# Performance work log

Measured on AMD Instinct MI355X. Metric: run time of the kernel, lower is better.

## Reference

```python
import jax, jax.numpy as jnp
import numpy as np

NUM_EXPERTS = 256
TOP_K = 8
N_GROUP = 8
TOPK_GROUP = 4
ROUTED_SCALING = 2.5
EXPERTS_PER_GROUP = NUM_EXPERTS // N_GROUP  # 32


def setup_inputs() -> dict:
    key = jax.random.key(0)
    k1, k2, k3 = jax.random.split(key, 3)
    hidden_states = jax.random.normal(k1, (8192, 7168), dtype=jnp.float32)
    weight = jax.random.normal(k2, (NUM_EXPERTS, 7168), dtype=jnp.float32) * 0.02
    e_score_correction_bias = jax.random.normal(k3, (NUM_EXPERTS,), dtype=jnp.float32) * 0.1
    return {
        "hidden_states": hidden_states,
        "weight": weight,
        "e_score_correction_bias": e_score_correction_bias,
    }


def reference(hidden_states, weight, e_score_correction_bias):
    # Router logits: [T, E]
    router_logits = jnp.einsum("th,eh->te", hidden_states, weight)
    scores = jax.nn.sigmoid(router_logits)
    scores_for_choice = scores + e_score_correction_bias  # [T, E]

    T = scores_for_choice.shape[0]
    # Group-limited selection (noaux_tc): group score = sum of top-2 experts in group
    grouped = scores_for_choice.reshape(T, N_GROUP, EXPERTS_PER_GROUP)
    group_top2, _ = jax.lax.top_k(grouped, 2)            # [T, G, 2]
    group_scores = group_top2.sum(axis=-1)               # [T, G]
    _, group_idx = jax.lax.top_k(group_scores, TOPK_GROUP)  # [T, topk_group]
    group_mask = jax.nn.one_hot(group_idx, N_GROUP, dtype=scores.dtype).max(axis=1)  # [T, G]
    expert_mask = jnp.repeat(group_mask, EXPERTS_PER_GROUP, axis=-1)  # [T, E]
    masked_scores = scores_for_choice * expert_mask

    # Final top-k experts; routing weights gathered from raw sigmoid scores
    _, selected_experts = jax.lax.top_k(masked_scores, TOP_K)         # [T, K] int32
    routing_weights = jnp.take_along_axis(scores, selected_experts, axis=-1)  # [T, K]
    routing_weights = routing_weights / (routing_weights.sum(axis=-1, keepdims=True) + 1e-20)
    routing_weights = routing_weights * ROUTED_SCALING
    return routing_weights, selected_experts
```

## Files before the change

### kernel.cpp

```cpp
#include <hip/hip_runtime.h>
#include <math.h>
#include <stdint.h>

#define T_TOK 8192
#define NEXP  256
#define HD    7168
#define PLANE ((size_t)T_TOK * NEXP)
#define SCALE 4096.0f
#define INV_S2 (1.0f / 16777216.0f)
#define BM 256
#define BK 32
#define NSTEP_TOT (HD / BK)
#define BIMG_STEP 32768

typedef _Float16 h8  __attribute__((ext_vector_type(8)));
typedef float f32x16 __attribute__((ext_vector_type(16)));
typedef __attribute__((address_space(3))) uint8_t       lds_t;
typedef __attribute__((address_space(1))) const uint8_t gbl_t;

__global__ __launch_bounds__(256) void wconv(const float* __restrict__ W,
                                             _Float16* __restrict__ img) {
  const int cc  = blockIdx.x * 256 + threadIdx.x;
  const int t   = cc >> 11;
  const int c   = cc & 2047;
  const int hl  = c >> 10;
  const int rem = c & 1023;
  const int row = rem >> 2;
  const int sp  = rem & 3;
  const int sl  = sp ^ ((row >> 1) & 3);
  const int k   = t * BK + sl * 8;

  const float* src = W + (size_t)row * HD + k;
  const float4 v0 = *(const float4*)src;
  const float4 v1 = *(const float4*)(src + 4);
  const float xs[8] = {v0.x, v0.y, v0.z, v0.w, v1.x, v1.y, v1.z, v1.w};
  h8 out;
#pragma unroll
  for (int j = 0; j < 8; ++j) {
    const float v = xs[j] * SCALE;
    const _Float16 hh = (_Float16)v;
    out[j] = hl ? (_Float16)(v - (float)hh) : hh;
  }
  *(h8*)(img + (size_t)cc * 8) = out;
}

__global__ __launch_bounds__(512, 2) void router_gemm(
    const float* __restrict__ X, const _Float16* __restrict__ img,
    float* __restrict__ partial, int S) {
  __shared__ __align__(1024) _Float16 As[2][2][BM][BK];
  __shared__ __align__(1024) _Float16 Bs[2][2][NEXP][BK];

  const int tid = threadIdx.x;
  const int id  = blockIdx.x;
  const int sb  = id % S;
  const int mb  = id / S;

  const int row0  = mb * BM;
  const int nstep = (HD / S) / BK;
  const int tbase = sb * nstep;

  const int lane = tid & 63, wv = tid >> 6;
  const int wm = wv >> 2, wn = wv & 3;
  const int r31 = lane & 31, kg = lane >> 5;

  const int sm = tid >> 1;
  const int sk = tid & 1;

  const float* Ap = X + (size_t)(row0 + sm) * HD + tbase * BK + sk * 16;
  const uint8_t* imgB = (const uint8_t*)img + (size_t)tbase * BIMG_STEP + tid * 16;

  f32x16 acc[4][2];
#pragma unroll
  for (int i = 0; i < 4; ++i)
#pragma unroll
    for (int j = 0; j < 2; ++j) acc[i][j] = (f32x16)(0.f);

#define LOAD_A(t)                                                              \
  {                                                                            \
    const float* ap = Ap + (size_t)(t) * BK;                                   \
    a0 = *(const float4*)(ap);                                                 \
    a1 = *(const float4*)(ap + 4);                                             \
    a2 = *(const float4*)(ap + 8);                                             \
    a3 = *(const float4*)(ap + 12);                                            \
  }

#define STAGE_B2(t, b, i0)                                                     \
  {                                                                            \
    const uint8_t* g = imgB + (size_t)(t) * BIMG_STEP;                         \
    uint8_t* l = (uint8_t*)&Bs[b][0][0][0] + tid * 16;                         \
    __builtin_amdgcn_global_load_lds((gbl_t*)(uintptr_t)(g + (i0) * 8192),     \
                                     (lds_t*)(uintptr_t)(l + (i0) * 8192), 16, 0, 0); \
    __builtin_amdgcn_global_load_lds((gbl_t*)(uintptr_t)(g + ((i0) + 1) * 8192), \
                                     (lds_t*)(uintptr_t)(l + ((i0) + 1) * 8192), 16, 0, 0); \
  }

#define CVT_WRITE_A(b)                                                         \
  {                                                                            \
    const float xs[16] = {a0.x, a0.y, a0.z, a0.w, a1.x, a1.y, a1.z, a1.w,      \
                          a2.x, a2.y, a2.z, a2.w, a3.x, a3.y, a3.z, a3.w};     \
    h8 hv0, hv1, lv0, lv1;                                                     \
    _Pragma("unroll")                                                          \
    for (int j = 0; j < 8; ++j) {                                              \
      const float v = xs[j] * SCALE;                                           \
      const _Float16 hh = (_Float16)v;                                         \
      hv0[j] = hh; lv0[j] = (_Float16)(v - (float)hh);                         \
    }                                                                          \
    _Pragma("unroll")                                                          \
    for (int j = 0; j < 8; ++j) {                                              \
      const float v = xs[8 + j] * SCALE;                                       \
      const _Float16 hh = (_Float16)v;                                         \
      hv1[j] = hh; lv1[j] = (_Float16)(v - (float)hh);                         \
    }                                                                          \
    const int s0 = (sk * 2) ^ ((sm >> 1) & 3);                                 \
    const int s1 = (sk * 2 + 1) ^ ((sm >> 1) & 3);                             \
    *(h8*)&As[b][0][sm][s0 * 8] = hv0;                                         \
    *(h8*)&As[b][0][sm][s1 * 8] = hv1;                                         \
    *(h8*)&As[b][1][sm][s0 * 8] = lv0;                                         \
    *(h8*)&As[b][1][sm][s1 * 8] = lv1;                                         \
  }

#define READ_B(ks, dst)                                                        \
  _Pragma("unroll")                                                            \
  for (int ni = 0; ni < 2; ++ni)                                               \
    _Pragma("unroll")                                                          \
    for (int pl = 0; pl < 2; ++pl) {                                           \
      const int col = wn * 64 + ni * 32 + r31;                                 \
      const int sp  = ((ks) * 2 + kg) ^ ((col >> 1) & 3);                      \
      dst[ni][pl] = *(const h8*)&Bs[cur][pl][col][sp * 8];                     \
    }

#define READ_A(ks, mbase, dst)                                                 \
  _Pragma("unroll")                                                            \
  for (int mi = 0; mi < 2; ++mi)                                               \
    _Pragma("unroll")                                                          \
    for (int pl = 0; pl < 2; ++pl) {                                           \
      const int row = wm * 128 + ((mbase) + mi) * 32 + r31;                    \
      const int sp  = ((ks) * 2 + kg) ^ ((row >> 1) & 3);                      \
      dst[mi][pl] = *(const h8*)&As[cur][pl][row][sp * 8];                     \
    }

#define MFMA12(aF, bF, mbase)                                                  \
  __builtin_amdgcn_s_setprio(1);                                               \
  _Pragma("unroll")                                                            \
  for (int mi = 0; mi < 2; ++mi)                                               \
    _Pragma("unroll")                                                          \
    for (int ni = 0; ni < 2; ++ni)                                             \
      acc[(mbase) + mi][ni] = __builtin_amdgcn_mfma_f32_32x32x16_f16(          \
          aF[mi][0], bF[ni][0], acc[(mbase) + mi][ni], 0, 0, 0);               \
  _Pragma("unroll")                                                            \
  for (int mi = 0; mi < 2; ++mi)                                               \
    _Pragma("unroll")                                                          \
    for (int ni = 0; ni < 2; ++ni)                                             \
      acc[(mbase) + mi][ni] = __builtin_amdgcn_mfma_f32_32x32x16_f16(          \
          aF[mi][1], bF[ni][0], acc[(mbase) + mi][ni], 0, 0, 0);               \
  _Pragma("unroll")                                                            \
  for (int mi = 0; mi < 2; ++mi)                                               \
    _Pragma("unroll")                                                          \
    for (int ni = 0; ni < 2; ++ni)                                             \
      acc[(mbase) + mi][ni] = __builtin_amdgcn_mfma_f32_32x32x16_f16(          \
          aF[mi][0], bF[ni][1], acc[(mbase) + mi][ni], 0, 0, 0);               \
  __builtin_amdgcn_s_setprio(0);

#define FENCE asm volatile("" ::: "memory");
#define BAR   __builtin_amdgcn_s_barrier();
#define WAITL0 asm volatile("s_waitcnt lgkmcnt(0)" ::: "memory"); __builtin_amdgcn_sched_barrier(0);

  {
    float4 a0, a1, a2, a3;
    LOAD_A(0);
    STAGE_B2(0, 0, 0);
    STAGE_B2(0, 0, 2);
    asm volatile("s_waitcnt vmcnt(4)" ::: "memory");
    CVT_WRITE_A(0);
    asm volatile("s_waitcnt vmcnt(0) lgkmcnt(0)" ::: "memory");
    BAR;
  }

  for (int t = 0; t < nstep; ++t) {
    const int cur = t & 1;
    const int nxt = cur ^ 1;
    const bool more = (t + 1 < nstep);

    h8 b0[2][2], b1[2][2], aA[2][2], aB[2][2];
    float4 a0, a1, a2, a3;

    READ_B(0, b0);
    READ_A(0, 0, aA);
    if (more) LOAD_A(t + 1);
    FENCE; BAR; WAITL0;
    MFMA12(aA, b0, 0);
    FENCE; BAR;

    READ_A(0, 2, aB);
    if (more) STAGE_B2(t + 1, nxt, 0);
    FENCE; BAR; WAITL0;
    MFMA12(aB, b0, 2);
    FENCE; BAR;

    READ_B(1, b1);
    READ_A(1, 0, aA);
    if (more) STAGE_B2(t + 1, nxt, 2);
    FENCE; BAR; WAITL0;
    MFMA12(aA, b1, 0);
    FENCE; BAR;

    READ_A(1, 2, aB);
    if (more) {
      asm volatile("s_waitcnt vmcnt(4)" ::: "memory");
      __builtin_amdgcn_sched_barrier(0);
      CVT_WRITE_A(nxt);
    }
    asm volatile("s_waitcnt lgkmcnt(0)" ::: "memory");
    __builtin_amdgcn_sched_barrier(0);
    BAR;
    MFMA12(aB, b1, 2);
    if (more) asm volatile("s_waitcnt vmcnt(0)" ::: "memory");
    FENCE; BAR;
  }

  float* base = partial + (size_t)sb * PLANE;
#pragma unroll
  for (int mi = 0; mi < 4; ++mi)
#pragma unroll
    for (int ni = 0; ni < 2; ++ni) {
      const int col = wn * 64 + ni * 32 + r31;
#pragma unroll
      for (int reg = 0; reg < 16; ++reg) {
        const int rr  = (reg & 3) + 8 * (reg >> 2) + 4 * kg;
        const int row = row0 + wm * 128 + mi * 32 + rr;
        base[(size_t)row * NEXP + col] = acc[mi][ni][reg];
      }
    }
}

__global__ __launch_bounds__(256) void gate_kernel(const float* __restrict__ logits,
                                                   const float* __restrict__ bias,
                                                   float* __restrict__ out_w,
                                                   float* __restrict__ out_e, int S) {
    const int wave = threadIdx.x >> 6;
    const int lane = threadIdx.x & 63;
    const int t = blockIdx.x * 4 + wave;
    if (t >= T_TOK) return;

    float l4[4] = {0.f, 0.f, 0.f, 0.f};
    for (int s = 0; s < S; ++s) {
        const float4 v = *(const float4*)(&logits[(size_t)s * PLANE + (size_t)t * NEXP + lane * 4]);
        l4[0] += v.x; l4[1] += v.y; l4[2] += v.z; l4[3] += v.w;
    }
    const float4 bv = *(const float4*)(&bias[lane * 4]);

    float s4[4], c[4];
#pragma unroll
    for (int j = 0; j < 4; ++j) s4[j] = 1.f / (1.f + expf(-l4[j] * INV_S2));
    c[0] = s4[0] + bv.x;
    c[1] = s4[1] + bv.y;
    c[2] = s4[2] + bv.z;
    c[3] = s4[3] + bv.w;

    float a = fmaxf(c[0], c[1]), b = fminf(c[0], c[1]);
    float d = fmaxf(c[2], c[3]), e = fminf(c[2], c[3]);
    float m1 = fmaxf(a, d);
    float m2 = fmaxf(fminf(a, d), fmaxf(b, e));
#pragma unroll
    for (int off = 1; off < 8; off <<= 1) {
        const float o1 = __shfl_xor(m1, off);
        const float o2 = __shfl_xor(m2, off);
        const float n1 = fmaxf(m1, o1);
        const float n2 = fmaxf(fminf(m1, o1), fmaxf(m2, o2));
        m1 = n1; m2 = n2;
    }
    const float gs = m1 + m2;
    const int   g  = lane >> 3;

    int rank = 0;
#pragma unroll
    for (int gg = 0; gg < 8; ++gg) {
        const float og = __shfl(gs, gg * 8);
        rank += (og > gs) || (og == gs && gg < g);
    }
    const bool gsel = rank < 4;

    float v[4];
#pragma unroll
    for (int j = 0; j < 4; ++j) v[j] = gsel ? c[j] : 0.0f;

    float selw = 0.f;
    int   seli = 0;
    float wsum = 0.f;

#pragma unroll
    for (int k = 0; k < 8; ++k) {
        float bvv = v[0]; int bi = lane * 4; float br = s4[0];
#pragma unroll
        for (int j = 1; j < 4; ++j) {
            if (v[j] > bvv) { bvv = v[j]; bi = lane * 4 + j; br = s4[j]; }
        }
#pragma unroll
        for (int off = 32; off > 0; off >>= 1) {
            const float ov = __shfl_xor(bvv, off);
            const int   oi = __shfl_xor(bi, off);
            const float orr = __shfl_xor(br, off);
            if (ov > bvv || (ov == bvv && oi < bi)) { bvv = ov; bi = oi; br = orr; }
        }
        if (lane == k) { selw = br; seli = bi; }
        wsum += br;
        const int rem = bi - lane * 4;
#pragma unroll
        for (int j = 0; j < 4; ++j)
            if (rem == j) v[j] = -INFINITY;
    }

    if (lane < 8) {
        const float w = selw / (wsum + 1e-20f) * 2.5f;
        out_w[(size_t)t * 8 + lane] = w;
        out_e[(size_t)t * 8 + lane] = (float)seli;
    }
}

extern "C" void kernel_launch(void* const* d_in, const int* in_sizes, int n_in,
                              void* d_out, int out_size, void* d_ws, size_t ws_size,
                              hipStream_t stream) {
    const float* X    = (const float*)d_in[0];
    const float* W    = (const float*)d_in[1];
    const float* bias = (const float*)d_in[2];
    float* out = (float*)d_out;

    _Float16* img = (_Float16*)d_ws;
    const size_t woff = (size_t)NSTEP_TOT * BIMG_STEP;
    float* partial = (float*)((char*)d_ws + woff);

    int S = 1;
    if (ws_size >= woff + 8 * PLANE * sizeof(float)) S = 8;
    else if (ws_size >= woff + 4 * PLANE * sizeof(float)) S = 4;
    else if (ws_size >= woff + 2 * PLANE * sizeof(float)) S = 2;

    wconv<<<dim3(NSTEP_TOT * 2048 / 256), 256, 0, stream>>>(W, img);
    router_gemm<<<dim3((T_TOK / BM) * S), 512, 0, stream>>>(X, img, partial, S);
    gate_kernel<<<dim3(T_TOK / 4), 256, 0, stream>>>(partial, bias, out, out + (size_t)T_TOK * 8, S);
}
```

Baseline: 135.2 us.

## Collapse per-step barriers into one and issue all LDS reads up front

Restructures the main GEMM k-loop so each step has a single workgroup barrier at the top instead of eight barrier points. All A and B fragment reads from LDS are issued early, and partial lgkmcnt waits interleave them with the four MFMA groups. The four B global-to-LDS loads are issued together in one batch. The aim is to cut barrier stalls and expose more overlap between LDS reads, global loads and MFMA work. In exchange it uses more fragment registers and depends on hand-counted waitcnt values being correct for the double-buffered LDS.

```diff
diff --git a/kernel.cpp b/kernel.cpp
--- a/kernel.cpp
+++ b/kernel.cpp
@@ -17,6 +17,8 @@
 typedef float f32x16 __attribute__((ext_vector_type(16)));
 typedef __attribute__((address_space(3))) uint8_t       lds_t;
 typedef __attribute__((address_space(1))) const uint8_t gbl_t;
+
+#define SB __builtin_amdgcn_sched_barrier(0);
 
 __global__ __launch_bounds__(256) void wconv(const float* __restrict__ W,
                                              _Float16* __restrict__ img) {
@@ -84,14 +86,14 @@
     a3 = *(const float4*)(ap + 12);                                            \
   }
 
-#define STAGE_B2(t, b, i0)                                                     \
+#define STAGE_B4(t, b)                                                         \
   {                                                                            \
     const uint8_t* g = imgB + (size_t)(t) * BIMG_STEP;                         \
     uint8_t* l = (uint8_t*)&Bs[b][0][0][0] + tid * 16;                         \
-    __builtin_amdgcn_global_load_lds((gbl_t*)(uintptr_t)(g + (i0) * 8192),     \
-                                     (lds_t*)(uintptr_t)(l + (i0) * 8192), 16, 0, 0); \
-    __builtin_amdgcn_global_load_lds((gbl_t*)(uintptr_t)(g + ((i0) + 1) * 8192), \
-                                     (lds_t*)(uintptr_t)(l + ((i0) + 1) * 8192), 16, 0, 0); \
+    _Pragma("unroll")                                                          \
+    for (int i = 0; i < 4; ++i)                                                \
+      __builtin_amdgcn_global_load_lds((gbl_t*)(uintptr_t)(g + i * 8192),      \
+                                       (lds_t*)(uintptr_t)(l + i * 8192), 16, 0, 0); \
   }
 
 #define CVT_WRITE_A(b)                                                         \
@@ -161,19 +163,12 @@
           aF[mi][0], bF[ni][1], acc[(mbase) + mi][ni], 0, 0, 0);               \
   __builtin_amdgcn_s_setprio(0);
 
-#define FENCE asm volatile("" ::: "memory");
-#define BAR   __builtin_amdgcn_s_barrier();
-#define WAITL0 asm volatile("s_waitcnt lgkmcnt(0)" ::: "memory"); __builtin_amdgcn_sched_barrier(0);
-
   {
     float4 a0, a1, a2, a3;
-    LOAD_A(0);
-    STAGE_B2(0, 0, 0);
-    STAGE_B2(0, 0, 2);
-    asm volatile("s_waitcnt vmcnt(4)" ::: "memory");
+    LOAD_A(0); SB;
+    STAGE_B4(0, 0); SB;
+    asm volatile("s_waitcnt vmcnt(4)" ::: "memory"); SB;
     CVT_WRITE_A(0);
-    asm volatile("s_waitcnt vmcnt(0) lgkmcnt(0)" ::: "memory");
-    BAR;
   }
 
   for (int t = 0; t < nstep; ++t) {
@@ -181,41 +176,42 @@
     const int nxt = cur ^ 1;
     const bool more = (t + 1 < nstep);
 
-    h8 b0[2][2], b1[2][2], aA[2][2], aB[2][2];
     float4 a0, a1, a2, a3;
+    h8 b0[2][2], b1[2][2], aP[2][2], aQ[2][2], aR[2][2], aS[2][2];
+
+    if (more) { LOAD_A(t + 1); }
+    SB;
+    if (more) { asm volatile("s_waitcnt vmcnt(2) lgkmcnt(0)" ::: "memory"); }
+    else      { asm volatile("s_waitcnt vmcnt(0) lgkmcnt(0)" ::: "memory"); }
+    SB;
+    __builtin_amdgcn_s_barrier();
 
     READ_B(0, b0);
-    READ_A(0, 0, aA);
-    if (more) LOAD_A(t + 1);
-    FENCE; BAR; WAITL0;
-    MFMA12(aA, b0, 0);
-    FENCE; BAR;
-
-    READ_A(0, 2, aB);
-    if (more) STAGE_B2(t + 1, nxt, 0);
-    FENCE; BAR; WAITL0;
-    MFMA12(aB, b0, 2);
-    FENCE; BAR;
-
+    READ_A(0, 0, aP);
+    READ_A(0, 2, aQ);
+    SB;
     READ_B(1, b1);
-    READ_A(1, 0, aA);
-    if (more) STAGE_B2(t + 1, nxt, 2);
-    FENCE; BAR; WAITL0;
-    MFMA12(aA, b1, 0);
-    FENCE; BAR;
-
-    READ_A(1, 2, aB);
+    SB;
+    if (more) { STAGE_B4(t + 1, nxt); }
+    SB;
+    asm volatile("s_waitcnt lgkmcnt(4)" ::: "memory"); SB;
+    MFMA12(aP, b0, 0);
+    SB;
+    READ_A(1, 0, aR);
+    READ_A(1, 2, aS);
+    SB;
+    MFMA12(aQ, b0, 2);
+    SB;
+    asm volatile("s_waitcnt lgkmcnt(4)" ::: "memory"); SB;
+    MFMA12(aR, b1, 0);
+    SB;
     if (more) {
-      asm volatile("s_waitcnt vmcnt(4)" ::: "memory");
-      __builtin_amdgcn_sched_barrier(0);
+      asm volatile("s_waitcnt vmcnt(4)" ::: "memory"); SB;
       CVT_WRITE_A(nxt);
-    }
-    asm volatile("s_waitcnt lgkmcnt(0)" ::: "memory");
-    __builtin_amdgcn_sched_barrier(0);
-    BAR;
-    MFMA12(aB, b1, 2);
-    if (more) asm volatile("s_waitcnt vmcnt(0)" ::: "memory");
-    FENCE; BAR;
+      SB;
+    }
+    asm volatile("s_waitcnt lgkmcnt(4)" ::: "memory"); SB;
+    MFMA12(aS, b1, 2);
   }
 
   float* base = partial + (size_t)sb * PLANE;
```

Result: slower. 140.5 us (+3.9%).
